# Performance work log

Hardware: AMD Instinct MI355X
Metric: run time of the kernel (lower is better)

## Reference

```python
import jax, jax.numpy as jnp
import numpy as np

N, D = 8192, 256

def _gram_rbf(x, y, sigma):
    x2 = jnp.sum(x * x, axis=-1)                      # [N]
    y2 = jnp.sum(y * y, axis=-1)                      # [M]
    xy = jnp.einsum('nd,md->nm', x, y)                # [N,M] GEMM
    sq = x2[:, None] + y2[None, :] - 2.0 * xy
    return jnp.exp(-sq / sigma)

def setup_inputs() -> dict:
    key = jax.random.key(0)
    k1, k2 = jax.random.split(key)
    return {
        'input': jax.random.normal(k1, (N, D), dtype=jnp.float32),
        'target': jax.random.normal(k2, (N, D), dtype=jnp.float32) + 0.5,
        'sigma': 256,
    }

def reference(input, target, sigma):
    XX = _gram_rbf(input, input, sigma)
    YY = _gram_rbf(target, target, sigma)
    XY = _gram_rbf(input, target, sigma)
    return jnp.mean(XX) + jnp.mean(YY) - 2.0 * jnp.mean(XY)
```

## Files before the change

kernel.cpp:

```cpp
#include <hip/hip_runtime.h>
#include <hip/hip_bf16.h>
#include <stdint.h>
#include <stddef.h>


#define N_PTS   8192
#define DIM     256
#define TWO_N   16384
#define CSTRIDE 16

#define AS1 __attribute__((address_space(1)))
#define AS3 __attribute__((address_space(3)))

typedef __attribute__((ext_vector_type(4))) float f32x4;
typedef __attribute__((ext_vector_type(4))) int   i32x4;
typedef __attribute__((ext_vector_type(8))) int   i32x8;

__global__ __launch_bounds__(256) void mmd_prep(const float* __restrict__ X,
                                                const float* __restrict__ Y,
                                                const int* __restrict__ sigmap,
                                                unsigned char* __restrict__ Zf8,
                                                float* __restrict__ n2,
                                                float* __restrict__ out) {
    if (blockIdx.x == 0 && threadIdx.x == 0) out[0] = 0.0f;

    const int wave = threadIdx.x >> 6;
    const int lane = threadIdx.x & 63;
    const int row  = blockIdx.x * 4 + wave;

    const float* src = (row < N_PTS) ? (X + (size_t)row * DIM)
                                     : (Y + (size_t)(row - N_PTS) * DIM);
    float4 v = ((const float4*)src)[lane];

    float s = v.x * v.x + v.y * v.y + v.z * v.z + v.w * v.w;
#pragma unroll
    for (int off = 32; off; off >>= 1) s += __shfl_down(s, off, 64);
    if (lane == 0) {
        const float c2 = -1.4426950408889634f / (float)(*sigmap);
        n2[row] = c2 * s;
    }

    const int p01 = __builtin_amdgcn_cvt_pk_fp8_f32(v.x, v.y, 0, false);
    const int p23 = __builtin_amdgcn_cvt_pk_fp8_f32(v.z, v.w, 0, false);
    const unsigned int pk = ((unsigned)p01 & 0xffffu) | ((unsigned)p23 << 16);
    *(unsigned int*)(Zf8 + (size_t)row * DIM + (size_t)lane * 4) = pk;
}

__global__ __launch_bounds__(256, 2) void mmd_main(const unsigned char* __restrict__ Zf8,
                                                   const float* __restrict__ n2,
                                                   const int* __restrict__ sigmap,
                                                   float* __restrict__ out) {
    __shared__ char smem_b[65536];
    __shared__ float wsum[4];

    const int bid = (int)blockIdx.x;
    const int br  = 127 - (bid >> 4);
    const int cc  = bid & 15;
    if (cc > br) return;

    const int t    = threadIdx.x;
    const int wave = t >> 6;
    const int lane = t & 63;
    const int wm   = wave >> 1;
    const int wn   = wave & 1;
    const int g    = lane >> 4;
    const int ml   = lane & 15;
    const int rowBase = br * 128;

    const float m2 = 2.8853900817779268f / (float)(*sigmap);
    const int   SC = 0x7f7f7f7f;

    {
        const int colBase0 = cc * 128;
#pragma unroll
        for (int i = 0; i < 8; ++i) {
            const int cidx = i * 256 + t;
            const int col  = cidx >> 4;
            const int s    = cidx & 15;
            const int gc   = s ^ (col & 15);
            const unsigned char* gp = Zf8 + (size_t)(colBase0 + col) * DIM + gc * 16;
            __builtin_amdgcn_global_load_lds((const AS1 void*)gp,
                                             (AS3 void*)(smem_b + (size_t)cidx * 16), 16, 0, 0);
        }
    }

    i32x8 af[4][2];
#pragma unroll
    for (int mt = 0; mt < 4; ++mt) {
        const unsigned char* rp =
            Zf8 + (size_t)(rowBase + wm * 64 + mt * 16 + ml) * DIM + g * 32;
#pragma unroll
        for (int kc = 0; kc < 2; ++kc) {
            union { i32x4 h[2]; i32x8 v; } u;
            u.h[0] = *(const i32x4*)(rp + kc * 128);
            u.h[1] = *(const i32x4*)(rp + kc * 128 + 16);
            af[mt][kc] = u.v;
        }
    }
    float a_i[4][4];
#pragma unroll
    for (int mt = 0; mt < 4; ++mt)
#pragma unroll
        for (int rr = 0; rr < 4; ++rr)
            a_i[mt][rr] = n2[rowBase + wm * 64 + mt * 16 + g * 4 + rr];

    float block_acc = 0.0f;
    const int brX = (br < 64);
    int cur = 0;

    for (int bc = cc; bc <= br; bc += CSTRIDE) {
        const int colBase = bc * 128;

        float b_j[4];
#pragma unroll
        for (int nt = 0; nt < 4; ++nt)
            b_j[nt] = n2[colBase + wn * 64 + nt * 16 + ml];

        f32x4 acc[4][4] = {};

        __syncthreads();

        if (bc + CSTRIDE <= br) {
            const int colBaseN = colBase + CSTRIDE * 128;
            char* dst = smem_b + (cur ^ 1) * 32768;
#pragma unroll
            for (int i = 0; i < 8; ++i) {
                const int cidx = i * 256 + t;
                const int col  = cidx >> 4;
                const int s    = cidx & 15;
                const int gc   = s ^ (col & 15);
                const unsigned char* gp = Zf8 + (size_t)(colBaseN + col) * DIM + gc * 16;
                __builtin_amdgcn_global_load_lds((const AS1 void*)gp,
                                                 (AS3 void*)(dst + (size_t)cidx * 16), 16, 0, 0);
            }
        }

        const char* buf = smem_b + cur * 32768;
#pragma unroll
        for (int kc = 0; kc < 2; ++kc) {
            const int j0 = kc * 8 + g * 2;
            i32x8 bf[4];
#pragma unroll
            for (int nt = 0; nt < 4; ++nt) {
                const int col = wn * 64 + nt * 16 + ml;
                const char* cb = buf + (size_t)col * 256;
                union { i32x4 h[2]; i32x8 v; } u;
                u.h[0] = *(const i32x4*)(cb + (size_t)((j0)     ^ ml) * 16);
                u.h[1] = *(const i32x4*)(cb + (size_t)((j0 + 1) ^ ml) * 16);
                bf[nt] = u.v;
            }
#pragma unroll
            for (int mt = 0; mt < 4; ++mt)
#pragma unroll
                for (int nt = 0; nt < 4; ++nt)
                    acc[mt][nt] = __builtin_amdgcn_mfma_scale_f32_16x16x128_f8f6f4(
                        af[mt][kc], bf[nt], acc[mt][nt],
                        0, 0,
                        0, SC,
                        0, SC);
        }

        float ts0 = 0.0f, ts1 = 0.0f, ts2 = 0.0f, ts3 = 0.0f;
#pragma unroll
        for (int mt = 0; mt < 4; ++mt)
#pragma unroll
            for (int nt = 0; nt < 4; ++nt) {
                const float ab = b_j[nt];
                ts0 += __builtin_amdgcn_exp2f(fmaf(acc[mt][nt][0], m2, a_i[mt][0] + ab));
                ts1 += __builtin_amdgcn_exp2f(fmaf(acc[mt][nt][1], m2, a_i[mt][1] + ab));
                ts2 += __builtin_amdgcn_exp2f(fmaf(acc[mt][nt][2], m2, a_i[mt][2] + ab));
                ts3 += __builtin_amdgcn_exp2f(fmaf(acc[mt][nt][3], m2, a_i[mt][3] + ab));
            }
        const float tsum = (ts0 + ts1) + (ts2 + ts3);

        const float sgn = ((bc < 64) == brX) ? 1.0f : -1.0f;
        const float w   = (bc == br) ? sgn : 2.0f * sgn;
        block_acc = fmaf(w, tsum, block_acc);
        cur ^= 1;
    }

    float s = block_acc;
#pragma unroll
    for (int off = 32; off; off >>= 1) s += __shfl_down(s, off, 64);
    if (lane == 0) wsum[wave] = s;
    __syncthreads();
    if (t == 0)
        atomicAdd(out, (wsum[0] + wsum[1] + wsum[2] + wsum[3]) * (1.0f / 67108864.0f));
}

extern "C" void kernel_launch(void* const* d_in, const int* in_sizes, int n_in,
                              void* d_out, int out_size, void* d_ws, size_t ws_size,
                              hipStream_t stream) {
    const float* X      = (const float*)d_in[0];
    const float* Y      = (const float*)d_in[1];
    const int*   sigmap = (const int*)d_in[2];
    float*       out    = (float*)d_out;

    unsigned char* Zf8 = (unsigned char*)d_ws;
    float*         n2  = (float*)((char*)d_ws + (size_t)TWO_N * DIM);

    mmd_prep<<<TWO_N / 4, 256, 0, stream>>>(X, Y, sigmap, Zf8, n2, out);
    mmd_main<<<128 * CSTRIDE, 256, 0, stream>>>(Zf8, n2, sigmap, out);
}
```

Baseline: 120.6 us.

## Halve column tile width to 64 and stage row norms in LDS for occupancy

Column tiles shrink from 128 to 64 wide, which halves the double-buffered LDS footprint and the per-wave accumulator registers, and the launch bound moves from 2 to 3 blocks per CU. Row norms are read from a small shared array instead of being held as 16 registers per thread. The triangular tiling and symmetric weighting are recomputed for the finer column granularity. The trade-off is more loop iterations, more syncs and less B-tile reuse per A fragment.

```diff
diff --git a/kernel.cpp b/kernel.cpp
--- a/kernel.cpp
+++ b/kernel.cpp
@@ -7,7 +7,7 @@
 #define N_PTS   8192
 #define DIM     256
 #define TWO_N   16384
-#define CSTRIDE 16
+#define CS2     16
 
 #define AS1 __attribute__((address_space(1)))
 #define AS3 __attribute__((address_space(3)))
@@ -46,17 +46,19 @@
     *(unsigned int*)(Zf8 + (size_t)row * DIM + (size_t)lane * 4) = pk;
 }
 
-__global__ __launch_bounds__(256, 2) void mmd_main(const unsigned char* __restrict__ Zf8,
+__global__ __launch_bounds__(256, 3) void mmd_main(const unsigned char* __restrict__ Zf8,
                                                    const float* __restrict__ n2,
                                                    const int* __restrict__ sigmap,
                                                    float* __restrict__ out) {
-    __shared__ char smem_b[65536];
+    __shared__ char smem_b[32768];
+    __shared__ float n2rS[128];
     __shared__ float wsum[4];
 
     const int bid = (int)blockIdx.x;
     const int br  = 127 - (bid >> 4);
-    const int cc  = bid & 15;
-    if (cc > br) return;
+    const int cs  = bid & (CS2 - 1);
+    const int bcMax = 2 * br + 1;
+    if (cs > bcMax) return;
 
     const int t    = threadIdx.x;
     const int wave = t >> 6;
@@ -71,9 +73,9 @@
     const int   SC = 0x7f7f7f7f;
 
     {
-        const int colBase0 = cc * 128;
-#pragma unroll
-        for (int i = 0; i < 8; ++i) {
+        const int colBase0 = cs * 64;
+#pragma unroll
+        for (int i = 0; i < 4; ++i) {
             const int cidx = i * 256 + t;
             const int col  = cidx >> 4;
             const int s    = cidx & 15;
@@ -83,6 +85,7 @@
                                              (AS3 void*)(smem_b + (size_t)cidx * 16), 16, 0, 0);
         }
     }
+    if (t < 128) n2rS[t] = n2[rowBase + t];
 
     i32x8 af[4][2];
 #pragma unroll
@@ -97,34 +100,28 @@
             af[mt][kc] = u.v;
         }
     }
-    float a_i[4][4];
-#pragma unroll
-    for (int mt = 0; mt < 4; ++mt)
-#pragma unroll
-        for (int rr = 0; rr < 4; ++rr)
-            a_i[mt][rr] = n2[rowBase + wm * 64 + mt * 16 + g * 4 + rr];
 
     float block_acc = 0.0f;
     const int brX = (br < 64);
     int cur = 0;
 
-    for (int bc = cc; bc <= br; bc += CSTRIDE) {
-        const int colBase = bc * 128;
-
-        float b_j[4];
-#pragma unroll
-        for (int nt = 0; nt < 4; ++nt)
-            b_j[nt] = n2[colBase + wn * 64 + nt * 16 + ml];
-
-        f32x4 acc[4][4] = {};
+    for (int bc = cs; bc <= bcMax; bc += CS2) {
+        const int colBase = bc * 64;
+
+        float b_j[2];
+#pragma unroll
+        for (int nt = 0; nt < 2; ++nt)
+            b_j[nt] = n2[colBase + wn * 32 + nt * 16 + ml];
+
+        f32x4 acc[4][2] = {};
 
         __syncthreads();
 
-        if (bc + CSTRIDE <= br) {
-            const int colBaseN = colBase + CSTRIDE * 128;
-            char* dst = smem_b + (cur ^ 1) * 32768;
-#pragma unroll
-            for (int i = 0; i < 8; ++i) {
+        if (bc + CS2 <= bcMax) {
+            const int colBaseN = colBase + CS2 * 64;
+            char* dst = smem_b + (cur ^ 1) * 16384;
+#pragma unroll
+            for (int i = 0; i < 4; ++i) {
                 const int cidx = i * 256 + t;
                 const int col  = cidx >> 4;
                 const int s    = cidx & 15;
@@ -135,24 +132,24 @@
             }
         }
 
-        const char* buf = smem_b + cur * 32768;
+        const char* buf = smem_b + cur * 16384;
 #pragma unroll
         for (int kc = 0; kc < 2; ++kc) {
             const int j0 = kc * 8 + g * 2;
-            i32x8 bf[4];
-#pragma unroll
-            for (int nt = 0; nt < 4; ++nt) {
-                const int col = wn * 64 + nt * 16 + ml;
+            i32x8 bf[2];
+#pragma unroll
+            for (int nt = 0; nt < 2; ++nt) {
+                const int col = wn * 32 + nt * 16 + ml;
                 const char* cb = buf + (size_t)col * 256;
                 union { i32x4 h[2]; i32x8 v; } u;
-                u.h[0] = *(const i32x4*)(cb + (size_t)((j0)     ^ ml) * 16);
-                u.h[1] = *(const i32x4*)(cb + (size_t)((j0 + 1) ^ ml) * 16);
+                u.h[0] = *(const i32x4*)(cb + (size_t)((j0)     ^ (col & 15)) * 16);
+                u.h[1] = *(const i32x4*)(cb + (size_t)((j0 + 1) ^ (col & 15)) * 16);
                 bf[nt] = u.v;
             }
 #pragma unroll
             for (int mt = 0; mt < 4; ++mt)
 #pragma unroll
-                for (int nt = 0; nt < 4; ++nt)
+                for (int nt = 0; nt < 2; ++nt)
                     acc[mt][nt] = __builtin_amdgcn_mfma_scale_f32_16x16x128_f8f6f4(
                         af[mt][kc], bf[nt], acc[mt][nt],
                         0, 0,
@@ -162,19 +159,21 @@
 
         float ts0 = 0.0f, ts1 = 0.0f, ts2 = 0.0f, ts3 = 0.0f;
 #pragma unroll
-        for (int mt = 0; mt < 4; ++mt)
-#pragma unroll
-            for (int nt = 0; nt < 4; ++nt) {
+        for (int mt = 0; mt < 4; ++mt) {
+            const f32x4 ar = *(const f32x4*)&n2rS[wm * 64 + mt * 16 + g * 4];
+#pragma unroll
+            for (int nt = 0; nt < 2; ++nt) {
                 const float ab = b_j[nt];
-                ts0 += __builtin_amdgcn_exp2f(fmaf(acc[mt][nt][0], m2, a_i[mt][0] + ab));
-                ts1 += __builtin_amdgcn_exp2f(fmaf(acc[mt][nt][1], m2, a_i[mt][1] + ab));
-                ts2 += __builtin_amdgcn_exp2f(fmaf(acc[mt][nt][2], m2, a_i[mt][2] + ab));
-                ts3 += __builtin_amdgcn_exp2f(fmaf(acc[mt][nt][3], m2, a_i[mt][3] + ab));
+                ts0 += __builtin_amdgcn_exp2f(fmaf(acc[mt][nt][0], m2, ar[0] + ab));
+                ts1 += __builtin_amdgcn_exp2f(fmaf(acc[mt][nt][1], m2, ar[1] + ab));
+                ts2 += __builtin_amdgcn_exp2f(fmaf(acc[mt][nt][2], m2, ar[2] + ab));
+                ts3 += __builtin_amdgcn_exp2f(fmaf(acc[mt][nt][3], m2, ar[3] + ab));
             }
+        }
         const float tsum = (ts0 + ts1) + (ts2 + ts3);
 
-        const float sgn = ((bc < 64) == brX) ? 1.0f : -1.0f;
-        const float w   = (bc == br) ? sgn : 2.0f * sgn;
+        const float sgn = ((bc < 128) == brX) ? 1.0f : -1.0f;
+        const float w   = (bc < 2 * br) ? 2.0f * sgn : sgn;
         block_acc = fmaf(w, tsum, block_acc);
         cur ^= 1;
     }
@@ -200,5 +199,5 @@
     float*         n2  = (float*)((char*)d_ws + (size_t)TWO_N * DIM);
 
     mmd_prep<<<TWO_N / 4, 256, 0, stream>>>(X, Y, sigmap, Zf8, n2, out);
-    mmd_main<<<128 * CSTRIDE, 256, 0, stream>>>(Zf8, n2, sigmap, out);
+    mmd_main<<<128 * CS2, 256, 0, stream>>>(Zf8, n2, sigmap, out);
 }
```

After: 122.9 us. About the same (+1.9%).
